# Kernel tuning notes

Hardware: AMD Instinct MI355X
Metric: run time of the kernel (lower is better)

## Reference

```python
import jax, jax.numpy as jnp
import numpy as np

N_PATCHES = 14
HIDDEN_D = 768
LN_EPS = 1e-5


def positional_embeddings(seq_len, d):
    # sin(i / 10000^(j/d)) for even j, cos(i / 10000^((j-1)/d)) for odd j
    i = jnp.arange(seq_len, dtype=jnp.float32)[:, None]
    j = jnp.arange(d, dtype=jnp.float32)[None, :]
    exponent = (jnp.floor(j / 2.0) * 2.0) / d
    angle = i / jnp.power(10000.0, exponent)
    return jnp.where(jnp.arange(d)[None, :] % 2 == 0, jnp.sin(angle), jnp.cos(angle))


def patchify(images, n_patches):
    # images: [B, C, H, W] -> patches: [B, n_patches^2, C*ph*pw]
    # flatten order per torch patch.flatten(): (C, ph, pw)
    B, C, H, W = images.shape
    ph, pw = H // n_patches, W // n_patches
    x = images.reshape(B, C, n_patches, ph, n_patches, pw)
    x = x.transpose(0, 2, 4, 1, 3, 5)  # [B, ny, nx, C, ph, pw]
    return x.reshape(B, n_patches * n_patches, C * ph * pw)


def setup_inputs() -> dict:
    key = jax.random.key(0)
    k_img, k_w, k_b, k_cls = jax.random.split(key, 4)
    B, C, H, W = 128, 3, 224, 224
    lin_in = (H // N_PATCHES) * (W // N_PATCHES) * C  # 768
    bound = 1.0 / np.sqrt(lin_in)
    return {
        "images": jax.random.normal(k_img, (B, C, H, W), dtype=jnp.float32),
        "W": jax.random.uniform(k_w, (HIDDEN_D, lin_in), jnp.float32, -bound, bound),
        "b": jax.random.uniform(k_b, (HIDDEN_D,), jnp.float32, -bound, bound),
        "class_token": jax.random.uniform(k_cls, (1, HIDDEN_D), jnp.float32),
        "gamma": jnp.ones((HIDDEN_D,), jnp.float32),
        "beta": jnp.zeros((HIDDEN_D,), jnp.float32),
    }


def reference(images, W, b, class_token, gamma, beta):
    B = images.shape[0]
    patches = patchify(images, N_PATCHES)                # [B, P^2, lin_in]
    tokens = jnp.einsum("bpi,di->bpd", patches, W) + b   # [B, P^2, D]
    cls = jnp.broadcast_to(class_token[None, :, :], (B, 1, HIDDEN_D))
    tokens = jnp.concatenate([cls, tokens], axis=1)      # [B, P^2+1, D]
    pos = positional_embeddings(N_PATCHES ** 2 + 1, HIDDEN_D)
    out = tokens + pos[None, :, :]
    mean = out.mean(axis=-1, keepdims=True)
    var = out.var(axis=-1, keepdims=True)
    out = (out - mean) / jnp.sqrt(var + LN_EPS)
    return out * gamma + beta
```

## Files before the change

kernel.cpp:

```cpp
#include <hip/hip_runtime.h>
#include <hip/hip_bf16.h>


#define IMG_B 128
#define IMG_C 3
#define IMG_HW 224
#define DTOK 768
#define NTOK 197
#define MROWS 25088

typedef __attribute__((ext_vector_type(4))) float f32x4;
typedef __attribute__((ext_vector_type(8))) short bf16x8;
typedef __attribute__((ext_vector_type(4))) short bf16x4;

__device__ __forceinline__ unsigned short f2b(float f) {
  union { float f; unsigned u; } v; v.f = f;
  unsigned u = v.u;
  return (unsigned short)((u + 0x7fffu + ((u >> 16) & 1u)) >> 16);
}

__device__ __forceinline__ void glds16(const void* g, void* l) {
  __builtin_amdgcn_global_load_lds(
      (const __attribute__((address_space(1))) unsigned int*)g,
      (__attribute__((address_space(3))) unsigned int*)l, 16, 0, 0);
}


__global__ void conv_w(const float* __restrict__ W, unsigned short* __restrict__ Wb) {
  int i = blockIdx.x * 256 + threadIdx.x;
  if (i < DTOK * DTOK) Wb[i] = f2b(W[i]);
}

__global__ void make_bpos(const float* __restrict__ bias, const float* __restrict__ cls,
                          float* __restrict__ bpos) {
  int i = blockIdx.x * 256 + threadIdx.x;
  if (i >= NTOK * DTOK) return;
  int t = i / DTOK, d = i - (i / DTOK) * DTOK;
  float expo = (float)(d & ~1) * (1.0f / (float)DTOK);
  float angle = (float)t * exp2f(-expo * 13.287712379549449f);
  float pv = (d & 1) ? cosf(angle) : sinf(angle);
  bpos[i] = pv + ((t == 0) ? cls[d] : bias[d]);
}

__global__ __launch_bounds__(256) void cls_kernel(const float* __restrict__ bpos,
                                                  const float* __restrict__ gamma,
                                                  const float* __restrict__ beta,
                                                  float* __restrict__ out) {
  __shared__ float sred[8];
  const int tid = threadIdx.x;
  float v0 = bpos[tid], v1 = bpos[tid + 256], v2 = bpos[tid + 512];
  float s1 = v0 + v1 + v2;
  float s2 = v0 * v0 + v1 * v1 + v2 * v2;
  #pragma unroll
  for (int off = 32; off >= 1; off >>= 1) {
    s1 += __shfl_xor(s1, off, 64);
    s2 += __shfl_xor(s2, off, 64);
  }
  if ((tid & 63) == 0) { sred[(tid >> 6) * 2] = s1; sred[(tid >> 6) * 2 + 1] = s2; }
  __syncthreads();
  float S1 = sred[0] + sred[2] + sred[4] + sred[6];
  float S2 = sred[1] + sred[3] + sred[5] + sred[7];
  float mean = S1 * (1.0f / 768.0f);
  float rstd = rsqrtf(S2 * (1.0f / 768.0f) - mean * mean + 1e-5f);
  float o0 = (v0 - mean) * rstd * gamma[tid] + beta[tid];
  float o1 = (v1 - mean) * rstd * gamma[tid + 256] + beta[tid + 256];
  float o2 = (v2 - mean) * rstd * gamma[tid + 512] + beta[tid + 512];
  for (int b = 0; b < IMG_B; ++b) {
    float* op = out + (size_t)b * NTOK * DTOK;
    op[tid] = o0; op[tid + 256] = o1; op[tid + 512] = o2;
  }
}


__global__ __launch_bounds__(512) void vit_main(
    const float* __restrict__ images, const unsigned short* __restrict__ Wb,
    const float* __restrict__ bpos, const float* __restrict__ gamma,
    const float* __restrict__ beta, float* __restrict__ out) {
  __shared__ unsigned short Bl[2][24576];
  __shared__ unsigned short Al[2][2048];
  __shared__ float red[8][64][2];
  __shared__ float rowstat[64][2];

  const int tid = threadIdx.x;
  const int wid = tid >> 6;
  const int lane = tid & 63;
  const int l15 = lane & 15;
  const int g = lane >> 4;
  const int blk = blockIdx.x;
  const int cbase = wid * 96;

  const int srow = tid >> 3;
  const int kq = tid & 7;
  const int sm = blk * 64 + srow;
  const int sb = sm / 196;
  const int sp = sm - sb * 196;
  const int spy = sp / 14, spx = sp - (sp / 14) * 14;
  const float* abase = images + (size_t)sb * (IMG_C * IMG_HW * IMG_HW) +
                       (spy * 16) * IMG_HW + spx * 16 + (kq & 3) * 4;
  const int bq = kq >> 2;
  const int aw_idx = (srow * 4 + ((kq >> 1) ^ ((srow >> 1) & 3))) * 8 + (kq & 1) * 4;

  int boff[6];
  #pragma unroll
  for (int j = 0; j < 6; ++j) {
    const int d = j * 512 + tid;
    const int r = d >> 2;
    const int q = (d & 3) ^ ((r >> 1) & 3);
    boff[j] = r * DTOK + q * 8;
  }
  const int bldsbase = wid * 512;

  const int sA = g ^ ((l15 >> 1) & 3);
  const int ard = l15 * 32 + sA * 8;
  const int brd = cbase * 32 + l15 * 32 + sA * 8;

  f32x4 acc[4][6];
  #pragma unroll
  for (int mf = 0; mf < 4; ++mf)
    #pragma unroll
    for (int nf = 0; nf < 6; ++nf)
      acc[mf][nf] = (f32x4)(0.0f);

  {
    const int v = bq;
    const float4 av = *(const float4*)(abase + (v >> 4) * 50176 + (v & 15) * 224);
    #pragma unroll
    for (int j = 0; j < 6; ++j)
      glds16(Wb + boff[j], &Bl[0][bldsbase + j * 4096]);
    union { __hip_bfloat162 h2[2]; bf16x4 v4; } u;
    u.h2[0] = __float22bfloat162_rn(make_float2(av.x, av.y));
    u.h2[1] = __float22bfloat162_rn(make_float2(av.z, av.w));
    *(bf16x4*)&Al[0][aw_idx] = u.v4;
    __syncthreads();
  }

  for (int k = 0; k < 24; ++k) {
    const int cur = k & 1, nxt = cur ^ 1;
    float4 av;
    if (k < 23) {
      const int v = (k + 1) * 2 + bq;
      av = *(const float4*)(abase + (v >> 4) * 50176 + (v & 15) * 224);
      #pragma unroll
      for (int j = 0; j < 6; ++j)
        glds16(Wb + boff[j] + (k + 1) * 32, &Bl[nxt][bldsbase + j * 4096]);
    }

    bf16x8 afr[4];
    #pragma unroll
    for (int mf = 0; mf < 4; ++mf)
      afr[mf] = *(const bf16x8*)&Al[cur][ard + mf * 512];

    #pragma unroll
    for (int nf = 0; nf < 6; ++nf) {
      const bf16x8 bf = *(const bf16x8*)&Bl[cur][brd + nf * 512];
      #pragma unroll
      for (int mf = 0; mf < 4; ++mf)
        acc[mf][nf] =
            __builtin_amdgcn_mfma_f32_16x16x32_bf16(afr[mf], bf, acc[mf][nf], 0, 0, 0);
    }

    if (k < 23) {
      union { __hip_bfloat162 h2[2]; bf16x4 v4; } u;
      u.h2[0] = __float22bfloat162_rn(make_float2(av.x, av.y));
      u.h2[1] = __float22bfloat162_rn(make_float2(av.z, av.w));
      *(bf16x4*)&Al[nxt][aw_idx] = u.v4;
    }
    __syncthreads();
  }

  float s1[16], s2[16];
  #pragma unroll
  for (int mf = 0; mf < 4; ++mf) {
    #pragma unroll
    for (int r = 0; r < 4; ++r) {
      const int rl = mf * 16 + g * 4 + r;
      const int m = blk * 64 + rl;
      const int trow = 1 + (m % 196);
      const float* bp = bpos + (size_t)trow * DTOK + cbase + l15;
      float a1 = 0.f, a2 = 0.f;
      #pragma unroll
      for (int nf = 0; nf < 6; ++nf) {
        float val = acc[mf][nf][r] + bp[nf * 16];
        acc[mf][nf][r] = val;
        a1 += val; a2 += val * val;
      }
      s1[mf * 4 + r] = a1; s2[mf * 4 + r] = a2;
    }
  }
  #pragma unroll
  for (int off = 8; off >= 1; off >>= 1) {
    #pragma unroll
    for (int i = 0; i < 16; ++i) {
      s1[i] += __shfl_xor(s1[i], off, 64);
      s2[i] += __shfl_xor(s2[i], off, 64);
    }
  }
  if (l15 == 0) {
    #pragma unroll
    for (int mf = 0; mf < 4; ++mf)
      #pragma unroll
      for (int r = 0; r < 4; ++r) {
        const int rl = mf * 16 + g * 4 + r;
        red[wid][rl][0] = s1[mf * 4 + r];
        red[wid][rl][1] = s2[mf * 4 + r];
      }
  }
  __syncthreads();
  if (tid < 64) {
    float S1 = 0.f, S2 = 0.f;
    #pragma unroll
    for (int w = 0; w < 8; ++w) { S1 += red[w][tid][0]; S2 += red[w][tid][1]; }
    float mean = S1 * (1.0f / 768.0f);
    float var = S2 * (1.0f / 768.0f) - mean * mean;
    rowstat[tid][0] = mean;
    rowstat[tid][1] = rsqrtf(var + 1e-5f);
  }
  __syncthreads();

  float gm[6], bt[6];
  #pragma unroll
  for (int nf = 0; nf < 6; ++nf) {
    gm[nf] = gamma[cbase + nf * 16 + l15];
    bt[nf] = beta[cbase + nf * 16 + l15];
  }
  #pragma unroll
  for (int mf = 0; mf < 4; ++mf) {
    #pragma unroll
    for (int r = 0; r < 4; ++r) {
      const int rl = mf * 16 + g * 4 + r;
      const int m = blk * 64 + rl;
      const int bb = m / 196;
      const int orow = bb * 197 + 1 + (m - bb * 196);
      const float mean = rowstat[rl][0], rstd = rowstat[rl][1];
      float* op = out + (size_t)orow * DTOK + cbase + l15;
      #pragma unroll
      for (int nf = 0; nf < 6; ++nf)
        op[nf * 16] = (acc[mf][nf][r] - mean) * rstd * gm[nf] + bt[nf];
    }
  }
}

extern "C" void kernel_launch(void* const* d_in, const int* in_sizes, int n_in,
                              void* d_out, int out_size, void* d_ws, size_t ws_size,
                              hipStream_t stream) {
  const float* images = (const float*)d_in[0];
  const float* W      = (const float*)d_in[1];
  const float* bias   = (const float*)d_in[2];
  const float* cls    = (const float*)d_in[3];
  const float* gamma  = (const float*)d_in[4];
  const float* beta   = (const float*)d_in[5];
  float* out = (float*)d_out;

  unsigned short* Wb = (unsigned short*)d_ws;
  float* bpos = (float*)((char*)d_ws + (size_t)DTOK * DTOK * 2);

  conv_w<<<(DTOK * DTOK + 255) / 256, 256, 0, stream>>>(W, Wb);
  make_bpos<<<(NTOK * DTOK + 255) / 256, 256, 0, stream>>>(bias, cls, bpos);
  cls_kernel<<<1, 256, 0, stream>>>(bpos, gamma, beta, out);
  vit_main<<<MROWS / 64, 512, 0, stream>>>(images, Wb, bpos, gamma, beta, out);
}
```

Baseline: 110.3 us.

## Load weight fragments directly from global into registers, dropping LDS B staging

```diff
diff --git a/kernel.cpp b/kernel.cpp
--- a/kernel.cpp
+++ b/kernel.cpp
@@ -17,12 +17,6 @@
   union { float f; unsigned u; } v; v.f = f;
   unsigned u = v.u;
   return (unsigned short)((u + 0x7fffu + ((u >> 16) & 1u)) >> 16);
-}
-
-__device__ __forceinline__ void glds16(const void* g, void* l) {
-  __builtin_amdgcn_global_load_lds(
-      (const __attribute__((address_space(1))) unsigned int*)g,
-      (__attribute__((address_space(3))) unsigned int*)l, 16, 0, 0);
 }
 
 
@@ -72,12 +66,11 @@
 }
 
 
-__global__ __launch_bounds__(512) void vit_main(
+__global__ __launch_bounds__(512, 2) void vit_main(
     const float* __restrict__ images, const unsigned short* __restrict__ Wb,
     const float* __restrict__ bpos, const float* __restrict__ gamma,
     const float* __restrict__ beta, float* __restrict__ out) {
-  __shared__ unsigned short Bl[2][24576];
-  __shared__ unsigned short Al[2][2048];
+  __shared__ __align__(16) unsigned short Al[2][2048];
   __shared__ float red[8][64][2];
   __shared__ float rowstat[64][2];
 
@@ -95,24 +88,17 @@
   const int sb = sm / 196;
   const int sp = sm - sb * 196;
   const int spy = sp / 14, spx = sp - (sp / 14) * 14;
+  const int bq = kq >> 2;
   const float* abase = images + (size_t)sb * (IMG_C * IMG_HW * IMG_HW) +
-                       (spy * 16) * IMG_HW + spx * 16 + (kq & 3) * 4;
-  const int bq = kq >> 2;
+                       (spy * 16) * IMG_HW + spx * 16 + (kq & 3) * 4 + bq * IMG_HW;
   const int aw_idx = (srow * 4 + ((kq >> 1) ^ ((srow >> 1) & 3))) * 8 + (kq & 1) * 4;
-
-  int boff[6];
-  #pragma unroll
-  for (int j = 0; j < 6; ++j) {
-    const int d = j * 512 + tid;
-    const int r = d >> 2;
-    const int q = (d & 3) ^ ((r >> 1) & 3);
-    boff[j] = r * DTOK + q * 8;
-  }
-  const int bldsbase = wid * 512;
-
   const int sA = g ^ ((l15 >> 1) & 3);
   const int ard = l15 * 32 + sA * 8;
-  const int brd = cbase * 32 + l15 * 32 + sA * 8;
+
+  const unsigned short* bbase[6];
+  #pragma unroll
+  for (int nf = 0; nf < 6; ++nf)
+    bbase[nf] = Wb + (size_t)(cbase + nf * 16 + l15) * DTOK + g * 8;
 
   f32x4 acc[4][6];
   #pragma unroll
@@ -121,52 +107,63 @@
     for (int nf = 0; nf < 6; ++nf)
       acc[mf][nf] = (f32x4)(0.0f);
 
+#define AOFF(t) (((t) >> 3) * 50176 + (((2 * (t)) & 15)) * 224)
+
+  float4 imgreg[2];
+  bf16x8 bfr[2][6];
+
   {
-    const int v = bq;
-    const float4 av = *(const float4*)(abase + (v >> 4) * 50176 + (v & 15) * 224);
-    #pragma unroll
-    for (int j = 0; j < 6; ++j)
-      glds16(Wb + boff[j], &Bl[0][bldsbase + j * 4096]);
+    const float4 a0 = *(const float4*)(abase + AOFF(0));
+    imgreg[1] = *(const float4*)(abase + AOFF(1));
+    #pragma unroll
+    for (int nf = 0; nf < 6; ++nf) {
+      bfr[0][nf] = *(const bf16x8*)(bbase[nf]);
+      bfr[1][nf] = *(const bf16x8*)(bbase[nf] + 32);
+    }
     union { __hip_bfloat162 h2[2]; bf16x4 v4; } u;
-    u.h2[0] = __float22bfloat162_rn(make_float2(av.x, av.y));
-    u.h2[1] = __float22bfloat162_rn(make_float2(av.z, av.w));
+    u.h2[0] = __float22bfloat162_rn(make_float2(a0.x, a0.y));
+    u.h2[1] = __float22bfloat162_rn(make_float2(a0.z, a0.w));
     *(bf16x4*)&Al[0][aw_idx] = u.v4;
-    __syncthreads();
-  }
-
+    asm volatile("s_waitcnt lgkmcnt(0)" ::: "memory");
+    __builtin_amdgcn_s_barrier();
+    __builtin_amdgcn_sched_barrier(0);
+  }
+
+  #pragma unroll
   for (int k = 0; k < 24; ++k) {
-    const int cur = k & 1, nxt = cur ^ 1;
-    float4 av;
-    if (k < 23) {
-      const int v = (k + 1) * 2 + bq;
-      av = *(const float4*)(abase + (v >> 4) * 50176 + (v & 15) * 224);
-      #pragma unroll
-      for (int j = 0; j < 6; ++j)
-        glds16(Wb + boff[j] + (k + 1) * 32, &Bl[nxt][bldsbase + j * 4096]);
-    }
+    if (k + 2 < 24)
+      imgreg[k & 1] = *(const float4*)(abase + AOFF(k + 2));
 
     bf16x8 afr[4];
     #pragma unroll
     for (int mf = 0; mf < 4; ++mf)
-      afr[mf] = *(const bf16x8*)&Al[cur][ard + mf * 512];
-
-    #pragma unroll
-    for (int nf = 0; nf < 6; ++nf) {
-      const bf16x8 bf = *(const bf16x8*)&Bl[cur][brd + nf * 512];
+      afr[mf] = *(const bf16x8*)&Al[k & 1][ard + mf * 512];
+
+    #pragma unroll
+    for (int nf = 0; nf < 6; ++nf)
       #pragma unroll
       for (int mf = 0; mf < 4; ++mf)
-        acc[mf][nf] =
-            __builtin_amdgcn_mfma_f32_16x16x32_bf16(afr[mf], bf, acc[mf][nf], 0, 0, 0);
-    }
-
-    if (k < 23) {
+        acc[mf][nf] = __builtin_amdgcn_mfma_f32_16x16x32_bf16(
+            afr[mf], bfr[k & 1][nf], acc[mf][nf], 0, 0, 0);
+
+    if (k + 2 < 24) {
+      #pragma unroll
+      for (int nf = 0; nf < 6; ++nf)
+        bfr[k & 1][nf] = *(const bf16x8*)(bbase[nf] + (k + 2) * 32);
+    }
+
+    if (k + 1 < 24) {
+      const float4 av = imgreg[(k + 1) & 1];
       union { __hip_bfloat162 h2[2]; bf16x4 v4; } u;
       u.h2[0] = __float22bfloat162_rn(make_float2(av.x, av.y));
       u.h2[1] = __float22bfloat162_rn(make_float2(av.z, av.w));
-      *(bf16x4*)&Al[nxt][aw_idx] = u.v4;
-    }
-    __syncthreads();
-  }
+      *(bf16x4*)&Al[(k + 1) & 1][aw_idx] = u.v4;
+    }
+    asm volatile("s_waitcnt lgkmcnt(0)" ::: "memory");
+    __builtin_amdgcn_s_barrier();
+    __builtin_amdgcn_sched_barrier(0);
+  }
+#undef AOFF
 
   float s1[16], s2[16];
   #pragma unroll
```

Result: slower. 114.5 us (+3.9%).

## Triple-buffer weight tiles in LDS and feed image fragments straight from registers

Applied to the files above, without the earlier changes.

```diff
diff --git a/kernel.cpp b/kernel.cpp
--- a/kernel.cpp
+++ b/kernel.cpp
@@ -11,12 +11,20 @@
 
 typedef __attribute__((ext_vector_type(4))) float f32x4;
 typedef __attribute__((ext_vector_type(8))) short bf16x8;
-typedef __attribute__((ext_vector_type(4))) short bf16x4;
 
 __device__ __forceinline__ unsigned short f2b(float f) {
   union { float f; unsigned u; } v; v.f = f;
   unsigned u = v.u;
   return (unsigned short)((u + 0x7fffu + ((u >> 16) & 1u)) >> 16);
+}
+
+__device__ __forceinline__ bf16x8 cvt8(float4 lo, float4 hi) {
+  union { __hip_bfloat162 h2[4]; bf16x8 v; } u;
+  u.h2[0] = __float22bfloat162_rn(make_float2(lo.x, lo.y));
+  u.h2[1] = __float22bfloat162_rn(make_float2(lo.z, lo.w));
+  u.h2[2] = __float22bfloat162_rn(make_float2(hi.x, hi.y));
+  u.h2[3] = __float22bfloat162_rn(make_float2(hi.z, hi.w));
+  return u.v;
 }
 
 __device__ __forceinline__ void glds16(const void* g, void* l) {
@@ -72,12 +80,11 @@
 }
 
 
-__global__ __launch_bounds__(512) void vit_main(
+__global__ __launch_bounds__(512, 2) void vit_main(
     const float* __restrict__ images, const unsigned short* __restrict__ Wb,
     const float* __restrict__ bpos, const float* __restrict__ gamma,
     const float* __restrict__ beta, float* __restrict__ out) {
-  __shared__ unsigned short Bl[2][24576];
-  __shared__ unsigned short Al[2][2048];
+  extern __shared__ unsigned short Bl[];
   __shared__ float red[8][64][2];
   __shared__ float rowstat[64][2];
 
@@ -86,19 +93,21 @@
   const int lane = tid & 63;
   const int l15 = lane & 15;
   const int g = lane >> 4;
-  const int blk = blockIdx.x;
+  const int blkraw = blockIdx.x;
+  const int blk = (blkraw & 7) * 49 + (blkraw >> 3);
   const int cbase = wid * 96;
-
-  const int srow = tid >> 3;
-  const int kq = tid & 7;
-  const int sm = blk * 64 + srow;
-  const int sb = sm / 196;
-  const int sp = sm - sb * 196;
-  const int spy = sp / 14, spx = sp - (sp / 14) * 14;
-  const float* abase = images + (size_t)sb * (IMG_C * IMG_HW * IMG_HW) +
-                       (spy * 16) * IMG_HW + spx * 16 + (kq & 3) * 4;
-  const int bq = kq >> 2;
-  const int aw_idx = (srow * 4 + ((kq >> 1) ^ ((srow >> 1) & 3))) * 8 + (kq & 1) * 4;
+  const int gb = g >> 1;
+
+  const float* abase[4];
+  #pragma unroll
+  for (int mf = 0; mf < 4; ++mf) {
+    const int m = blk * 64 + mf * 16 + l15;
+    const int sb = m / 196;
+    const int sp = m - sb * 196;
+    const int spy = sp / 14, spx = sp - (sp / 14) * 14;
+    abase[mf] = images + (size_t)sb * (IMG_C * IMG_HW * IMG_HW) +
+                (spy * 16) * IMG_HW + spx * 16 + (g & 1) * 8;
+  }
 
   int boff[6];
   #pragma unroll
@@ -109,9 +118,7 @@
     boff[j] = r * DTOK + q * 8;
   }
   const int bldsbase = wid * 512;
-
   const int sA = g ^ ((l15 >> 1) & 3);
-  const int ard = l15 * 32 + sA * 8;
   const int brd = cbase * 32 + l15 * 32 + sA * 8;
 
   f32x4 acc[4][6];
@@ -121,52 +128,71 @@
     for (int nf = 0; nf < 6; ++nf)
       acc[mf][nf] = (f32x4)(0.0f);
 
+  float4 aimg[2][8];
+
+#define AOFF(T) ((((2 * (T) + 0) >> 4)) * 50176)
+
   {
-    const int v = bq;
-    const float4 av = *(const float4*)(abase + (v >> 4) * 50176 + (v & 15) * 224);
+    const int idx0 = gb;
+    const int ao = (idx0 >> 4) * 50176 + (idx0 & 15) * 224;
+    #pragma unroll
+    for (int mf = 0; mf < 4; ++mf) {
+      aimg[0][mf * 2]     = *(const float4*)(abase[mf] + ao);
+      aimg[0][mf * 2 + 1] = *(const float4*)(abase[mf] + ao + 4);
+    }
+    asm volatile("" ::: "memory");
     #pragma unroll
     for (int j = 0; j < 6; ++j)
-      glds16(Wb + boff[j], &Bl[0][bldsbase + j * 4096]);
-    union { __hip_bfloat162 h2[2]; bf16x4 v4; } u;
-    u.h2[0] = __float22bfloat162_rn(make_float2(av.x, av.y));
-    u.h2[1] = __float22bfloat162_rn(make_float2(av.z, av.w));
-    *(bf16x4*)&Al[0][aw_idx] = u.v4;
-    __syncthreads();
-  }
-
-  for (int k = 0; k < 24; ++k) {
-    const int cur = k & 1, nxt = cur ^ 1;
-    float4 av;
-    if (k < 23) {
-      const int v = (k + 1) * 2 + bq;
-      av = *(const float4*)(abase + (v >> 4) * 50176 + (v & 15) * 224);
-      #pragma unroll
-      for (int j = 0; j < 6; ++j)
-        glds16(Wb + boff[j] + (k + 1) * 32, &Bl[nxt][bldsbase + j * 4096]);
-    }
-
-    bf16x8 afr[4];
-    #pragma unroll
-    for (int mf = 0; mf < 4; ++mf)
-      afr[mf] = *(const bf16x8*)&Al[cur][ard + mf * 512];
-
-    #pragma unroll
-    for (int nf = 0; nf < 6; ++nf) {
-      const bf16x8 bf = *(const bf16x8*)&Bl[cur][brd + nf * 512];
-      #pragma unroll
-      for (int mf = 0; mf < 4; ++mf)
-        acc[mf][nf] =
-            __builtin_amdgcn_mfma_f32_16x16x32_bf16(afr[mf], bf, acc[mf][nf], 0, 0, 0);
-    }
-
-    if (k < 23) {
-      union { __hip_bfloat162 h2[2]; bf16x4 v4; } u;
-      u.h2[0] = __float22bfloat162_rn(make_float2(av.x, av.y));
-      u.h2[1] = __float22bfloat162_rn(make_float2(av.z, av.w));
-      *(bf16x4*)&Al[nxt][aw_idx] = u.v4;
-    }
-    __syncthreads();
-  }
+      glds16(Wb + boff[j], Bl + 0 * 24576 + bldsbase + j * 4096);
+    #pragma unroll
+    for (int j = 0; j < 6; ++j)
+      glds16(Wb + boff[j] + 32, Bl + 1 * 24576 + bldsbase + j * 4096);
+    asm volatile("" ::: "memory");
+  }
+
+#define STEP(K, CNT)                                                           \
+  {                                                                            \
+    asm volatile("s_waitcnt vmcnt(" CNT ")" ::: "memory");                     \
+    __builtin_amdgcn_s_barrier();                                              \
+    if ((K) + 1 < 24) {                                                        \
+      const int idxn_ = 2 * ((K) + 1) + gb;                                    \
+      const int aon_ = (idxn_ >> 4) * 50176 + (idxn_ & 15) * 224;              \
+      _Pragma("unroll")                                                        \
+      for (int mf = 0; mf < 4; ++mf) {                                         \
+        aimg[((K) + 1) & 1][mf * 2]     = *(const float4*)(abase[mf] + aon_);  \
+        aimg[((K) + 1) & 1][mf * 2 + 1] = *(const float4*)(abase[mf] + aon_ + 4); \
+      }                                                                        \
+    }                                                                          \
+    if ((K) + 2 < 24) {                                                        \
+      _Pragma("unroll")                                                        \
+      for (int j = 0; j < 6; ++j)                                              \
+        glds16(Wb + boff[j] + ((K) + 2) * 32,                                  \
+               Bl + (((K) + 2) % 3) * 24576 + bldsbase + j * 4096);            \
+    }                                                                          \
+    asm volatile("" ::: "memory");                                             \
+    bf16x8 afr[4];                                                             \
+    _Pragma("unroll")                                                          \
+    for (int mf = 0; mf < 4; ++mf)                                             \
+      afr[mf] = cvt8(aimg[(K) & 1][mf * 2], aimg[(K) & 1][mf * 2 + 1]);        \
+    _Pragma("unroll")                                                          \
+    for (int nf = 0; nf < 6; ++nf) {                                           \
+      const bf16x8 bf =                                                        \
+          *(const bf16x8*)(Bl + ((K) % 3) * 24576 + brd + nf * 512);           \
+      _Pragma("unroll")                                                        \
+      for (int mf = 0; mf < 4; ++mf)                                           \
+        acc[mf][nf] = __builtin_amdgcn_mfma_f32_16x16x32_bf16(                 \
+            afr[mf], bf, acc[mf][nf], 0, 0, 0);                                \
+    }                                                                          \
+  }
+
+  STEP(0, "0")
+  STEP(1, "14")  STEP(2, "14")  STEP(3, "14")  STEP(4, "14")
+  STEP(5, "14")  STEP(6, "14")  STEP(7, "14")  STEP(8, "14")
+  STEP(9, "14")  STEP(10, "14") STEP(11, "14") STEP(12, "14")
+  STEP(13, "14") STEP(14, "14") STEP(15, "14") STEP(16, "14")
+  STEP(17, "14") STEP(18, "14") STEP(19, "14") STEP(20, "14")
+  STEP(21, "14") STEP(22, "14") STEP(23, "8")
+#undef STEP
 
   float s1[16], s2[16];
   #pragma unroll
@@ -195,6 +221,7 @@
       s2[i] += __shfl_xor(s2[i], off, 64);
     }
   }
+  __syncthreads();
   if (l15 == 0) {
     #pragma unroll
     for (int mf = 0; mf < 4; ++mf)
@@ -257,5 +284,5 @@
   conv_w<<<(DTOK * DTOK + 255) / 256, 256, 0, stream>>>(W, Wb);
   make_bpos<<<(NTOK * DTOK + 255) / 256, 256, 0, stream>>>(bias, cls, bpos);
   cls_kernel<<<1, 256, 0, stream>>>(bpos, gamma, beta, out);
-  vit_main<<<MROWS / 64, 512, 0, stream>>>(images, Wb, bpos, gamma, beta, out);
-}
+  vit_main<<<MROWS / 64, 512, 147456, stream>>>(images, Wb, bpos, gamma, beta, out);
+}
```

Result: slower. 130.1 us (+18.0%).
